# Performance work log

Measured on AMD Instinct MI355X. Metric: run time of the kernel, lower is better.

The kernel has to match this reference:

```python
import jax, jax.numpy as jnp
import numpy as np

BN_EPS = 1e-5


def setup_inputs() -> dict:
    key = jax.random.key(0)
    ks = jax.random.split(key, 9)
    C = 256
    x = jax.random.normal(ks[0], (4, C, 56, 56), jnp.float32)
    Wq = jax.random.normal(ks[1], (C // 4, C), jnp.float32) * 0.05
    Wk = jax.random.normal(ks[2], (C // 4, C), jnp.float32) * 0.05
    Wv = jax.random.normal(ks[3], (C, 2 * C), jnp.float32) * 0.05
    bv = jax.random.normal(ks[4], (C,), jnp.float32) * 0.05
    gamma = jnp.ones((C,), jnp.float32)
    beta = jnp.zeros((C,), jnp.float32)
    rmean = jax.random.normal(ks[5], (C,), jnp.float32) * 0.05
    rvar = jax.random.uniform(ks[6], (C,), jnp.float32) + 0.5
    return {"x": x, "Wq": Wq, "Wk": Wk, "Wv": Wv, "bv": bv,
            "gamma": gamma, "beta": beta, "rmean": rmean, "rvar": rvar, "k": 7}


def _patches(t, k):
    # t: [b, c, h, w] -> [b, c, k*k, h, w], zero-padded neighborhoods (matches F.unfold row-major order)
    b, c, h, w = t.shape
    p = (k - 1) // 2
    tp = jnp.pad(t, ((0, 0), (0, 0), (p, p), (p, p)))
    return jnp.stack([tp[:, :, i:i + h, j:j + w] for i in range(k) for j in range(k)], axis=2)


def _align(ta, tb, k, Wq, Wk):
    b, c, h, w = ta.shape
    hw = h * w
    # query token per pixel: [b, hw, 1, c]
    spta = ta.reshape(b, c, hw).transpose(0, 2, 1)[:, :, None, :]
    # unfolded k^2 neighborhood of tb: [b, hw, k2, c]
    pt = _patches(tb, k).reshape(b, c, k * k, hw).transpose(0, 3, 2, 1)
    keys = jnp.concatenate([spta, pt], axis=2)          # [b, hw, 1+k2, c]
    q = jnp.einsum('bnqc,dc->bnqd', spta, Wq)           # [b, hw, 1, c/4]
    kk = jnp.einsum('bnkc,dc->bnkd', keys, Wk)          # [b, hw, 1+k2, c/4]
    attn = jax.nn.softmax(jnp.einsum('bnqd,bnkd->bnqk', q, kk), axis=-1)
    out = jnp.einsum('bnqk,bnkc->bnqc', attn[..., 1:], pt)  # drop self-key column
    return out[:, :, 0, :].transpose(0, 2, 1).reshape(b, c, h, w)


def reference(x, Wq, Wk, Wv, bv, gamma, beta, rmean, rvar, k):
    xt1, xt2 = jnp.split(x, 2, axis=0)
    xt1 = _align(xt2, xt1, k, Wq, Wk)   # note: second call uses the freshly aligned xt1 (as in source)
    xt2 = _align(xt1, xt2, k, Wq, Wk)
    xt = jnp.concatenate([xt1, xt2], axis=0)
    cat = jnp.concatenate([x, xt], axis=1)              # [2B, 2C, H, W]
    y = jnp.einsum('bchw,oc->bohw', cat, Wv) + bv[None, :, None, None]
    scale = (gamma / jnp.sqrt(rvar + BN_EPS))[None, :, None, None]
    y = (y - rmean[None, :, None, None]) * scale + beta[None, :, None, None]
    return jax.nn.relu(y)
```

## Files before the change

### kernel.cpp

```cpp
#include <hip/hip_runtime.h>
#include <hip/hip_bf16.h>

#define HW 3136
#define W56 56

typedef __attribute__((ext_vector_type(8))) short short8;
typedef __attribute__((ext_vector_type(4))) float f32x4;

static __device__ __forceinline__ f32x4 mfma16(short8 a, short8 b, f32x4 c) {
    return __builtin_amdgcn_mfma_f32_16x16x32_bf16(a, b, c, 0, 0, 0);
}
static __device__ __forceinline__ float b2f(unsigned short u) {
    unsigned int x = ((unsigned int)u) << 16;
    return __builtin_bit_cast(float, x);
}
static __device__ __forceinline__ unsigned short f2b(float f) {
    __hip_bfloat16 h = __float2bfloat16(f);
    return *(unsigned short*)&h;
}

__global__ __launch_bounds__(256) void prep(const float* __restrict__ x,
                                            const float* __restrict__ Wq, const float* __restrict__ Wk,
                                            const float* __restrict__ Wv,
                                            unsigned short* __restrict__ catb,
                                            unsigned short* __restrict__ xlo,
                                            unsigned short* __restrict__ Wqk_hi,
                                            unsigned short* __restrict__ Wqk_lo,
                                            unsigned short* __restrict__ Wvb) {
    __shared__ float tile[32][33];
    int bx = blockIdx.x, tid = threadIdx.x;
    if (bx < 3136) {
        int b = bx / 784, rem = bx % 784;
        int p0 = (rem >> 3) * 32, c0 = (rem & 7) * 32;
        int tx = tid & 31, ty = tid >> 5;
#pragma unroll
        for (int i = ty; i < 32; i += 8)
            tile[i][tx] = x[((size_t)b * 256 + c0 + i) * HW + p0 + tx];
        __syncthreads();
#pragma unroll
        for (int i = ty; i < 32; i += 8) {
            float v = tile[tx][i];
            unsigned short hi = f2b(v);
            unsigned short lo = f2b(v - b2f(hi));
            size_t row = (size_t)b * HW + p0 + i;
            catb[row * 512 + c0 + tx] = hi;
            xlo[row * 256 + c0 + tx] = lo;
        }
    } else {
        int i = (bx - 3136) * 256 + tid;
        if (i < 32768) {
            float w = (i < 16384) ? Wq[i] : Wk[i - 16384];
            unsigned short hi = f2b(w);
            Wqk_hi[i] = hi;
            Wqk_lo[i] = f2b(w - b2f(hi));
        }
        if (i < 131072) Wvb[i] = f2b(Wv[i]);
    }
}

__global__ __launch_bounds__(256) void projqk(const unsigned short* __restrict__ Whi,
                                              const unsigned short* __restrict__ Wlo,
                                              const unsigned short* __restrict__ Bhi_g, int bstr,
                                              const unsigned short* __restrict__ Blo_g,
                                              float* __restrict__ Qout, float* __restrict__ Kout) {
    __shared__ short Ahi[64][72], Alo[64][72];
    __shared__ short Bhi[32][72], Blo[32][72];
    int tid = threadIdx.x, lane = tid & 63, wv = tid >> 6;
    int l15 = lane & 15, lk = (lane >> 4) * 8;
    int pxb = blockIdx.x * 32;
    int y64 = blockIdx.y * 64;
    f32x4 acc[2];
    acc[0] = (f32x4){0.f, 0.f, 0.f, 0.f};
    acc[1] = (f32x4){0.f, 0.f, 0.f, 0.f};

    for (int kt = 0; kt < 256; kt += 64) {
#pragma unroll
        for (int s = 0; s < 2; ++s) {
            int q = tid + 256 * s;
            int r = q >> 3, c = (q & 7) * 8;
            *(short8*)&Ahi[r][c] = *(const short8*)(Whi + (size_t)(y64 + r) * 256 + kt + c);
            *(short8*)&Alo[r][c] = *(const short8*)(Wlo + (size_t)(y64 + r) * 256 + kt + c);
        }
        {
            int r = tid >> 3, c = (tid & 7) * 8;
            *(short8*)&Bhi[r][c] = *(const short8*)(Bhi_g + (size_t)(pxb + r) * bstr + kt + c);
            *(short8*)&Blo[r][c] = *(const short8*)(Blo_g + (size_t)(pxb + r) * 256 + kt + c);
        }
        __syncthreads();
#pragma unroll
        for (int ks = 0; ks < 2; ++ks) {
            short8 ah = *(const short8*)&Ahi[wv * 16 + l15][ks * 32 + lk];
            short8 al = *(const short8*)&Alo[wv * 16 + l15][ks * 32 + lk];
            short8 bh[2], bl[2];
#pragma unroll
            for (int j = 0; j < 2; ++j) {
                bh[j] = *(const short8*)&Bhi[j * 16 + l15][ks * 32 + lk];
                bl[j] = *(const short8*)&Blo[j * 16 + l15][ks * 32 + lk];
            }
#pragma unroll
            for (int j = 0; j < 2; ++j) {
                acc[j] = mfma16(ah, bh[j], acc[j]);
                acc[j] = mfma16(ah, bl[j], acc[j]);
                acc[j] = mfma16(al, bh[j], acc[j]);
            }
        }
        __syncthreads();
    }
    int d0 = wv * 16 + (lane >> 4) * 4;
    float* base = blockIdx.y ? Kout : Qout;
#pragma unroll
    for (int j = 0; j < 2; ++j) {
        int px = pxb + j * 16 + l15;
        *(f32x4*)(base + (size_t)px * 64 + d0) = acc[j];
    }
}

__global__ __launch_bounds__(256) void attn_kernel(const float* __restrict__ Q,
                                                   const float* __restrict__ Kbase,
                                                   int selfOff, int kbOff,
                                                   const unsigned short* __restrict__ V,
                                                   unsigned short* __restrict__ outb,
                                                   unsigned short* __restrict__ outlo) {
    __shared__ float qs[4][64];
    __shared__ float wsh[4][64];
    __shared__ float ls[4][52];
    __shared__ int njsh[4][64];
    int tid = threadIdx.x, lane = tid & 63, wv = tid >> 6;
    int nbc = gridDim.x >> 3;
    int lb = (blockIdx.x & 7) * nbc + (blockIdx.x >> 3);
    int gw = lb * 4 + wv;
    int b = gw / HW, pix = gw % HW;
    int py = pix / W56, px = pix % W56;
    qs[wv][lane] = Q[(size_t)gw * 64 + lane];

    int valid = 0, nj = 0;
    if (lane == 0) {
        valid = 1;
    } else if (lane < 50) {
        int d = lane - 1, dy = d / 7 - 3, dx = d % 7 - 3;
        int ny = py + dy, nx = px + dx;
        if (ny >= 0 && ny < W56 && nx >= 0 && nx < W56) { valid = 1; nj = ny * W56 + nx; }
    }
    njsh[wv][lane] = nj;
    unsigned long long vmask = __ballot(lane < 50 && valid);
    __syncthreads();

    int rg = lane >> 4, c = lane & 15;
    f32x4 qf = *(const f32x4*)&qs[wv][c * 4];
    float4 kvv[13];
#pragma unroll
    for (int i = 0; i < 13; ++i) {
        int r = i * 4 + rg;
        int row = (i == 0 && rg == 0) ? (selfOff + gw) : (kbOff + b * HW + njsh[wv][r]);
        kvv[i] = *(const float4*)(Kbase + (size_t)row * 64 + c * 4);
    }
    float pl[13];
#pragma unroll
    for (int i = 0; i < 13; ++i)
        pl[i] = kvv[i].x * qf[0] + kvv[i].y * qf[1] + kvv[i].z * qf[2] + kvv[i].w * qf[3];
#pragma unroll
    for (int off = 1; off < 16; off <<= 1)
#pragma unroll
        for (int i = 0; i < 13; ++i) pl[i] += __shfl_xor(pl[i], off);
    float myl = 0.f;
#pragma unroll
    for (int i = 0; i < 13; ++i) myl = (c == i) ? pl[i] : myl;
    if (c < 13) ls[wv][c * 4 + rg] = myl;

    bool ok = (lane == 0) || (lane < 50 && ((vmask >> lane) & 1ull));
    float logit = (lane < 50 && ok) ? ls[wv][lane] : 0.f;
    float m = (lane < 50) ? logit : -1e30f;
#pragma unroll
    for (int off = 32; off; off >>= 1) m = fmaxf(m, __shfl_xor(m, off));
    float e = (lane < 50) ? __expf(logit - m) : 0.f;
    float s = e;
#pragma unroll
    for (int off = 32; off; off >>= 1) s += __shfl_xor(s, off);
    float w = (lane >= 1 && lane < 50 && valid) ? e / s : 0.f;
    wsh[wv][lane] = w;
    __syncthreads();

    int h = lane >> 5, l32 = lane & 31;
    int jb = h * 25;
    float av[8];
#pragma unroll
    for (int cc = 0; cc < 8; ++cc) av[cc] = 0.f;
    const unsigned short* vb = V + (size_t)b * HW * 512 + l32 * 8;
#pragma unroll
    for (int g = 0; g < 2; ++g) {
        float wj[12];
        short8 vj[12];
#pragma unroll
        for (int u = 0; u < 12; ++u) {
            int j = jb + g * 12 + u;
            wj[u] = wsh[wv][j];
            vj[u] = *(const short8*)(vb + (size_t)njsh[wv][j] * 512);
        }
#pragma unroll
        for (int u = 0; u < 12; ++u)
#pragma unroll
            for (int cc = 0; cc < 8; ++cc)
                av[cc] += wj[u] * b2f((unsigned short)vj[u][cc]);
    }
    {
        int j = jb + 24;
        float wt = wsh[wv][j];
        short8 vt = *(const short8*)(vb + (size_t)njsh[wv][j] * 512);
#pragma unroll
        for (int cc = 0; cc < 8; ++cc) av[cc] += wt * b2f((unsigned short)vt[cc]);
    }
#pragma unroll
    for (int cc = 0; cc < 8; ++cc) av[cc] += __shfl_xor(av[cc], 32);

    if (h == 0) {
        short8 pk, lo8;
#pragma unroll
        for (int cc = 0; cc < 8; ++cc) {
            unsigned short hi = f2b(av[cc]);
            pk[cc] = (short)hi;
            lo8[cc] = (short)f2b(av[cc] - b2f(hi));
        }
        *(short8*)(outb + (size_t)gw * 512 + l32 * 8) = pk;
        if (outlo) *(short8*)(outlo + (size_t)gw * 256 + l32 * 8) = lo8;
    }
}

__global__ __launch_bounds__(256) void conv_mfma(const unsigned short* __restrict__ catb,
                                                 const unsigned short* __restrict__ Wvb,
                                                 const float* __restrict__ bv, const float* __restrict__ gamma,
                                                 const float* __restrict__ beta, const float* __restrict__ rmean,
                                                 const float* __restrict__ rvar, float* __restrict__ out) {
    __shared__ short Ald[64][72];
    __shared__ short Bld[64][72];
    int tid = threadIdx.x, lane = tid & 63, wv = tid >> 6;
    int wm = wv >> 1, wn = wv & 1;
    int l15 = lane & 15, lk = (lane >> 4) * 8;
    int n0g = blockIdx.x * 64;
    int m0g = blockIdx.y * 64;
    f32x4 acc[2][2];
#pragma unroll
    for (int i = 0; i < 2; ++i)
#pragma unroll
        for (int j = 0; j < 2; ++j) acc[i][j] = (f32x4){0.f, 0.f, 0.f, 0.f};

    float sc_[2][4], sh_[2][4];
#pragma unroll
    for (int i = 0; i < 2; ++i) {
        int ob = m0g + wm * 32 + i * 16 + (lane >> 4) * 4;
#pragma unroll
        for (int r = 0; r < 4; ++r) {
            int o = ob + r;
            float s = gamma[o] * rsqrtf(rvar[o] + 1e-5f);
            sc_[i][r] = s;
            sh_[i][r] = (bv[o] - rmean[o]) * s + beta[o];
        }
    }

    for (int kt = 0; kt < 512; kt += 64) {
#pragma unroll
        for (int s = 0; s < 2; ++s) {
            int q = tid + 256 * s;
            int r = q >> 3, c = (q & 7) * 8;
            *(short8*)&Ald[r][c] = *(const short8*)(Wvb + (size_t)(m0g + r) * 512 + kt + c);
            *(short8*)&Bld[r][c] = *(const short8*)(catb + (size_t)(n0g + r) * 512 + kt + c);
        }
        __syncthreads();
#pragma unroll
        for (int ks = 0; ks < 2; ++ks) {
            short8 a[2], b[2];
#pragma unroll
            for (int i = 0; i < 2; ++i) a[i] = *(const short8*)&Ald[wm * 32 + i * 16 + l15][ks * 32 + lk];
#pragma unroll
            for (int j = 0; j < 2; ++j) b[j] = *(const short8*)&Bld[wn * 32 + j * 16 + l15][ks * 32 + lk];
#pragma unroll
            for (int i = 0; i < 2; ++i)
#pragma unroll
                for (int j = 0; j < 2; ++j) acc[i][j] = mfma16(a[i], b[j], acc[i][j]);
        }
        __syncthreads();
    }
#pragma unroll
    for (int i = 0; i < 2; ++i) {
        int ob = m0g + wm * 32 + i * 16 + (lane >> 4) * 4;
#pragma unroll
        for (int j = 0; j < 2; ++j) {
            int px = n0g + wn * 32 + j * 16 + l15;
            int b = px / HW, p = px - b * HW;
            f32x4 v = acc[i][j];
#pragma unroll
            for (int r = 0; r < 4; ++r) {
                out[((size_t)(b * 256 + ob + r)) * HW + p] = fmaxf(v[r] * sc_[i][r] + sh_[i][r], 0.f);
            }
        }
    }
}

extern "C" void kernel_launch(void* const* d_in, const int* in_sizes, int n_in,
                              void* d_out, int out_size, void* d_ws, size_t ws_size,
                              hipStream_t stream) {
    const float* x     = (const float*)d_in[0];
    const float* Wq    = (const float*)d_in[1];
    const float* Wk    = (const float*)d_in[2];
    const float* Wv    = (const float*)d_in[3];
    const float* bv    = (const float*)d_in[4];
    const float* gamma = (const float*)d_in[5];
    const float* beta  = (const float*)d_in[6];
    const float* rmean = (const float*)d_in[7];
    const float* rvar  = (const float*)d_in[8];
    float* out = (float*)d_out;

    float* Qall = (float*)d_ws;
    float* Kall = Qall + (size_t)4 * HW * 64;
    float* Qn   = Kall + (size_t)4 * HW * 64;
    float* Kn   = Qn + (size_t)2 * HW * 64;
    unsigned short* catb   = (unsigned short*)(Kn + (size_t)2 * HW * 64);
    unsigned short* xlo    = catb + (size_t)4 * HW * 512;
    unsigned short* xt1lo  = xlo + (size_t)4 * HW * 256;
    unsigned short* Wqk_hi = xt1lo + (size_t)2 * HW * 256;
    unsigned short* Wqk_lo = Wqk_hi + 128 * 256;
    unsigned short* Wvb    = Wqk_lo + 128 * 256;

    prep<<<3648, 256, 0, stream>>>(x, Wq, Wk, Wv, catb, xlo, Wqk_hi, Wqk_lo, Wvb);

    projqk<<<dim3(392, 2), 256, 0, stream>>>(Wqk_hi, Wqk_lo, catb, 512, xlo, Qall, Kall);

    attn_kernel<<<1568, 256, 0, stream>>>(Qall + (size_t)2 * HW * 64, Kall,
                                          2 * HW, 0,
                                          catb, catb + 256, xt1lo);

    projqk<<<dim3(196, 2), 256, 0, stream>>>(Wqk_hi, Wqk_lo, catb + 256, 512, xt1lo, Qn, Kn);

    attn_kernel<<<1568, 256, 0, stream>>>(Qn, Kall,
                                          6 * HW, 2 * HW,
                                          catb + (size_t)2 * HW * 512,
                                          catb + (size_t)2 * HW * 512 + 256, nullptr);

    conv_mfma<<<dim3(196, 4), 256, 0, stream>>>(catb, Wvb, bv, gamma, beta, rmean, rvar, out);
}
```

Measured before the change: 65.40 us.

## Stage shared V neighborhood tile in LDS for four adjacent pixels per block

Each block's four pixels are adjacent in a row, so their 7x7 neighborhoods are loaded once as a 7x10 tile of V rows into shared memory. The per-wave gathers then read from LDS instead of global memory. The Q staging in LDS and the first barrier are dropped, and the V loads are issued before the softmax to overlap latency. This costs about 35 KB of LDS per block, which may reduce occupancy.

```diff
diff --git a/kernel.cpp b/kernel.cpp
--- a/kernel.cpp
+++ b/kernel.cpp
@@ -121,32 +121,37 @@
                                                    const unsigned short* __restrict__ V,
                                                    unsigned short* __restrict__ outb,
                                                    unsigned short* __restrict__ outlo) {
-    __shared__ float qs[4][64];
+    __shared__ unsigned short Vs[70 * 256];
     __shared__ float wsh[4][64];
     __shared__ float ls[4][52];
     __shared__ int njsh[4][64];
+    __shared__ int slotsh[4][64];
     int tid = threadIdx.x, lane = tid & 63, wv = tid >> 6;
     int nbc = gridDim.x >> 3;
     int lb = (blockIdx.x & 7) * nbc + (blockIdx.x >> 3);
-    int gw = lb * 4 + wv;
-    int b = gw / HW, pix = gw % HW;
-    int py = pix / W56, px = pix % W56;
-    qs[wv][lane] = Q[(size_t)gw * 64 + lane];
-
-    int valid = 0, nj = 0;
+    int pixg = lb * 4;
+    int b = pixg / HW, pix0 = pixg % HW;
+    int row0 = pix0 / W56, px0 = pix0 % W56;
+    int gw = pixg + wv;
+    int py = row0, px = px0 + wv;
+
+    int valid = 0, nj = 0, slot = 0;
     if (lane == 0) {
         valid = 1;
     } else if (lane < 50) {
         int d = lane - 1, dy = d / 7 - 3, dx = d % 7 - 3;
         int ny = py + dy, nx = px + dx;
-        if (ny >= 0 && ny < W56 && nx >= 0 && nx < W56) { valid = 1; nj = ny * W56 + nx; }
+        if (ny >= 0 && ny < W56 && nx >= 0 && nx < W56) {
+            valid = 1;
+            nj = ny * W56 + nx;
+            slot = (dy + 3) * 10 + (wv + dx + 3);
+        }
     }
     njsh[wv][lane] = nj;
-    unsigned long long vmask = __ballot(lane < 50 && valid);
-    __syncthreads();
+    slotsh[wv][lane] = slot;
 
     int rg = lane >> 4, c = lane & 15;
-    f32x4 qf = *(const f32x4*)&qs[wv][c * 4];
+    f32x4 qf = *(const f32x4*)(Q + (size_t)gw * 64 + c * 4);
     float4 kvv[13];
 #pragma unroll
     for (int i = 0; i < 13; ++i) {
@@ -154,6 +159,21 @@
         int row = (i == 0 && rg == 0) ? (selfOff + gw) : (kbOff + b * HW + njsh[wv][r]);
         kvv[i] = *(const float4*)(Kbase + (size_t)row * 64 + c * 4);
     }
+
+    const unsigned short* Vb = V + (size_t)b * HW * 512;
+    short8 svj[9];
+#pragma unroll
+    for (int it = 0; it < 9; ++it) {
+        int item = it * 256 + tid;
+        if (item < 2240) {
+            int urow = item >> 5, sl = item & 31;
+            int r = urow / 10, cc = urow % 10;
+            int ny = row0 - 3 + r, nx = px0 - 3 + cc;
+            int unj = (ny >= 0 && ny < W56 && nx >= 0 && nx < W56) ? (ny * W56 + nx) : 0;
+            svj[it] = *(const short8*)(Vb + (size_t)unj * 512 + sl * 8);
+        }
+    }
+
     float pl[13];
 #pragma unroll
     for (int i = 0; i < 13; ++i)
@@ -167,8 +187,7 @@
     for (int i = 0; i < 13; ++i) myl = (c == i) ? pl[i] : myl;
     if (c < 13) ls[wv][c * 4 + rg] = myl;
 
-    bool ok = (lane == 0) || (lane < 50 && ((vmask >> lane) & 1ull));
-    float logit = (lane < 50 && ok) ? ls[wv][lane] : 0.f;
+    float logit = (lane < 50 && valid) ? ls[wv][lane] : 0.f;
     float m = (lane < 50) ? logit : -1e30f;
 #pragma unroll
     for (int off = 32; off; off >>= 1) m = fmaxf(m, __shfl_xor(m, off));
@@ -178,6 +197,15 @@
     for (int off = 32; off; off >>= 1) s += __shfl_xor(s, off);
     float w = (lane >= 1 && lane < 50 && valid) ? e / s : 0.f;
     wsh[wv][lane] = w;
+
+#pragma unroll
+    for (int it = 0; it < 9; ++it) {
+        int item = it * 256 + tid;
+        if (item < 2240) {
+            int urow = item >> 5, sl = item & 31;
+            *(short8*)&Vs[urow * 256 + sl * 8] = svj[it];
+        }
+    }
     __syncthreads();
 
     int h = lane >> 5, l32 = lane & 31;
@@ -185,7 +213,6 @@
     float av[8];
 #pragma unroll
     for (int cc = 0; cc < 8; ++cc) av[cc] = 0.f;
-    const unsigned short* vb = V + (size_t)b * HW * 512 + l32 * 8;
 #pragma unroll
     for (int g = 0; g < 2; ++g) {
         float wj[12];
@@ -194,7 +221,7 @@
         for (int u = 0; u < 12; ++u) {
             int j = jb + g * 12 + u;
             wj[u] = wsh[wv][j];
-            vj[u] = *(const short8*)(vb + (size_t)njsh[wv][j] * 512);
+            vj[u] = *(const short8*)&Vs[slotsh[wv][j] * 256 + l32 * 8];
         }
 #pragma unroll
         for (int u = 0; u < 12; ++u)
@@ -205,7 +232,7 @@
     {
         int j = jb + 24;
         float wt = wsh[wv][j];
-        short8 vt = *(const short8*)(vb + (size_t)njsh[wv][j] * 512);
+        short8 vt = *(const short8*)&Vs[slotsh[wv][j] * 256 + l32 * 8];
 #pragma unroll
         for (int cc = 0; cc < 8; ++cc) av[cc] += wt * b2f((unsigned short)vt[cc]);
     }
```

Result: slower. 68.34 us (+4.5%).

## Store K projections as bf16, prefetch projqk tiles, drop attn block barriers

Applied to the files above, without the earlier changes.

The K projection output is now written as bf16 instead of fp32, and the attention kernel gathers these half-size rows for the 49-neighbour dot products. This halves the bytes moved by the main gather. projqk now prefetches the next K-tile into registers while the MFMAs run on the current shared-memory tile. The attention kernel reads Q straight from global memory and drops its two __syncthreads, relying on each wave touching only its own shared rows. Rounding K to bf16 reduces logit precision, which may slightly change the softmax weights.

```diff
diff --git a/kernel.cpp b/kernel.cpp
--- a/kernel.cpp
+++ b/kernel.cpp
@@ -62,31 +62,42 @@
                                               const unsigned short* __restrict__ Wlo,
                                               const unsigned short* __restrict__ Bhi_g, int bstr,
                                               const unsigned short* __restrict__ Blo_g,
-                                              float* __restrict__ Qout, float* __restrict__ Kout) {
+                                              float* __restrict__ Qout,
+                                              unsigned short* __restrict__ Kout) {
     __shared__ short Ahi[64][72], Alo[64][72];
     __shared__ short Bhi[32][72], Blo[32][72];
     int tid = threadIdx.x, lane = tid & 63, wv = tid >> 6;
     int l15 = lane & 15, lk = (lane >> 4) * 8;
     int pxb = blockIdx.x * 32;
     int y64 = blockIdx.y * 64;
+    int ar0 = tid >> 3, ac = (tid & 7) * 8;
+    int br = tid >> 3, bc = (tid & 7) * 8;
     f32x4 acc[2];
     acc[0] = (f32x4){0.f, 0.f, 0.f, 0.f};
     acc[1] = (f32x4){0.f, 0.f, 0.f, 0.f};
 
-    for (int kt = 0; kt < 256; kt += 64) {
-#pragma unroll
-        for (int s = 0; s < 2; ++s) {
-            int q = tid + 256 * s;
-            int r = q >> 3, c = (q & 7) * 8;
-            *(short8*)&Ahi[r][c] = *(const short8*)(Whi + (size_t)(y64 + r) * 256 + kt + c);
-            *(short8*)&Alo[r][c] = *(const short8*)(Wlo + (size_t)(y64 + r) * 256 + kt + c);
-        }
-        {
-            int r = tid >> 3, c = (tid & 7) * 8;
-            *(short8*)&Bhi[r][c] = *(const short8*)(Bhi_g + (size_t)(pxb + r) * bstr + kt + c);
-            *(short8*)&Blo[r][c] = *(const short8*)(Blo_g + (size_t)(pxb + r) * 256 + kt + c);
-        }
-        __syncthreads();
+    short8 rAh0 = *(const short8*)(Whi + (size_t)(y64 + ar0) * 256 + ac);
+    short8 rAl0 = *(const short8*)(Wlo + (size_t)(y64 + ar0) * 256 + ac);
+    short8 rAh1 = *(const short8*)(Whi + (size_t)(y64 + ar0 + 32) * 256 + ac);
+    short8 rAl1 = *(const short8*)(Wlo + (size_t)(y64 + ar0 + 32) * 256 + ac);
+    short8 rBh  = *(const short8*)(Bhi_g + (size_t)(pxb + br) * bstr + bc);
+    short8 rBl  = *(const short8*)(Blo_g + (size_t)(pxb + br) * 256 + bc);
+
+#pragma unroll
+    for (int t = 0; t < 4; ++t) {
+        *(short8*)&Ahi[ar0][ac] = rAh0;      *(short8*)&Alo[ar0][ac] = rAl0;
+        *(short8*)&Ahi[ar0 + 32][ac] = rAh1; *(short8*)&Alo[ar0 + 32][ac] = rAl1;
+        *(short8*)&Bhi[br][bc] = rBh;        *(short8*)&Blo[br][bc] = rBl;
+        __syncthreads();
+        if (t < 3) {
+            int kn = t * 64 + 64;
+            rAh0 = *(const short8*)(Whi + (size_t)(y64 + ar0) * 256 + kn + ac);
+            rAl0 = *(const short8*)(Wlo + (size_t)(y64 + ar0) * 256 + kn + ac);
+            rAh1 = *(const short8*)(Whi + (size_t)(y64 + ar0 + 32) * 256 + kn + ac);
+            rAl1 = *(const short8*)(Wlo + (size_t)(y64 + ar0 + 32) * 256 + kn + ac);
+            rBh  = *(const short8*)(Bhi_g + (size_t)(pxb + br) * bstr + kn + bc);
+            rBl  = *(const short8*)(Blo_g + (size_t)(pxb + br) * 256 + kn + bc);
+        }
 #pragma unroll
         for (int ks = 0; ks < 2; ++ks) {
             short8 ah = *(const short8*)&Ahi[wv * 16 + l15][ks * 32 + lk];
@@ -107,21 +118,30 @@
         __syncthreads();
     }
     int d0 = wv * 16 + (lane >> 4) * 4;
-    float* base = blockIdx.y ? Kout : Qout;
-#pragma unroll
-    for (int j = 0; j < 2; ++j) {
-        int px = pxb + j * 16 + l15;
-        *(f32x4*)(base + (size_t)px * 64 + d0) = acc[j];
+    if (blockIdx.y == 0) {
+#pragma unroll
+        for (int j = 0; j < 2; ++j) {
+            int px = pxb + j * 16 + l15;
+            *(f32x4*)(Qout + (size_t)px * 64 + d0) = acc[j];
+        }
+    } else {
+#pragma unroll
+        for (int j = 0; j < 2; ++j) {
+            int px = pxb + j * 16 + l15;
+            ushort4 kb;
+            kb.x = f2b(acc[j][0]); kb.y = f2b(acc[j][1]);
+            kb.z = f2b(acc[j][2]); kb.w = f2b(acc[j][3]);
+            *(ushort4*)(Kout + (size_t)px * 64 + d0) = kb;
+        }
     }
 }
 
 __global__ __launch_bounds__(256) void attn_kernel(const float* __restrict__ Q,
-                                                   const float* __restrict__ Kbase,
+                                                   const unsigned short* __restrict__ Kb,
                                                    int selfOff, int kbOff,
                                                    const unsigned short* __restrict__ V,
                                                    unsigned short* __restrict__ outb,
                                                    unsigned short* __restrict__ outlo) {
-    __shared__ float qs[4][64];
     __shared__ float wsh[4][64];
     __shared__ float ls[4][52];
     __shared__ int njsh[4][64];
@@ -131,7 +151,6 @@
     int gw = lb * 4 + wv;
     int b = gw / HW, pix = gw % HW;
     int py = pix / W56, px = pix % W56;
-    qs[wv][lane] = Q[(size_t)gw * 64 + lane];
 
     int valid = 0, nj = 0;
     if (lane == 0) {
@@ -142,22 +161,22 @@
         if (ny >= 0 && ny < W56 && nx >= 0 && nx < W56) { valid = 1; nj = ny * W56 + nx; }
     }
     njsh[wv][lane] = nj;
-    unsigned long long vmask = __ballot(lane < 50 && valid);
-    __syncthreads();
 
     int rg = lane >> 4, c = lane & 15;
-    f32x4 qf = *(const f32x4*)&qs[wv][c * 4];
-    float4 kvv[13];
+    f32x4 qf = *(const f32x4*)(Q + (size_t)gw * 64 + c * 4);
+    ushort4 kvv[13];
 #pragma unroll
     for (int i = 0; i < 13; ++i) {
         int r = i * 4 + rg;
         int row = (i == 0 && rg == 0) ? (selfOff + gw) : (kbOff + b * HW + njsh[wv][r]);
-        kvv[i] = *(const float4*)(Kbase + (size_t)row * 64 + c * 4);
-    }
+        kvv[i] = *(const ushort4*)(Kb + (size_t)row * 64 + c * 4);
+    }
+
     float pl[13];
 #pragma unroll
     for (int i = 0; i < 13; ++i)
-        pl[i] = kvv[i].x * qf[0] + kvv[i].y * qf[1] + kvv[i].z * qf[2] + kvv[i].w * qf[3];
+        pl[i] = b2f(kvv[i].x) * qf[0] + b2f(kvv[i].y) * qf[1] +
+                b2f(kvv[i].z) * qf[2] + b2f(kvv[i].w) * qf[3];
 #pragma unroll
     for (int off = 1; off < 16; off <<= 1)
 #pragma unroll
@@ -167,8 +186,7 @@
     for (int i = 0; i < 13; ++i) myl = (c == i) ? pl[i] : myl;
     if (c < 13) ls[wv][c * 4 + rg] = myl;
 
-    bool ok = (lane == 0) || (lane < 50 && ((vmask >> lane) & 1ull));
-    float logit = (lane < 50 && ok) ? ls[wv][lane] : 0.f;
+    float logit = (lane < 50 && valid) ? ls[wv][lane] : 0.f;
     float m = (lane < 50) ? logit : -1e30f;
 #pragma unroll
     for (int off = 32; off; off >>= 1) m = fmaxf(m, __shfl_xor(m, off));
@@ -178,7 +196,6 @@
     for (int off = 32; off; off >>= 1) s += __shfl_xor(s, off);
     float w = (lane >= 1 && lane < 50 && valid) ? e / s : 0.f;
     wsh[wv][lane] = w;
-    __syncthreads();
 
     int h = lane >> 5, l32 = lane & 31;
     int jb = h * 25;
@@ -310,10 +327,9 @@
     float* out = (float*)d_out;
 
     float* Qall = (float*)d_ws;
-    float* Kall = Qall + (size_t)4 * HW * 64;
-    float* Qn   = Kall + (size_t)4 * HW * 64;
-    float* Kn   = Qn + (size_t)2 * HW * 64;
-    unsigned short* catb   = (unsigned short*)(Kn + (size_t)2 * HW * 64);
+    float* Qn   = Qall + (size_t)4 * HW * 64;
+    unsigned short* Kb = (unsigned short*)(Qn + (size_t)2 * HW * 64);
+    unsigned short* catb   = Kb + (size_t)6 * HW * 64;
     unsigned short* xlo    = catb + (size_t)4 * HW * 512;
     unsigned short* xt1lo  = xlo + (size_t)4 * HW * 256;
     unsigned short* Wqk_hi = xt1lo + (size_t)2 * HW * 256;
@@ -322,16 +338,17 @@
 
     prep<<<3648, 256, 0, stream>>>(x, Wq, Wk, Wv, catb, xlo, Wqk_hi, Wqk_lo, Wvb);
 
-    projqk<<<dim3(392, 2), 256, 0, stream>>>(Wqk_hi, Wqk_lo, catb, 512, xlo, Qall, Kall);
-
-    attn_kernel<<<1568, 256, 0, stream>>>(Qall + (size_t)2 * HW * 64, Kall,
+    projqk<<<dim3(392, 2), 256, 0, stream>>>(Wqk_hi, Wqk_lo, catb, 512, xlo, Qall, Kb);
+
+    attn_kernel<<<1568, 256, 0, stream>>>(Qall + (size_t)2 * HW * 64, Kb,
                                           2 * HW, 0,
                                           catb, catb + 256, xt1lo);
 
-    projqk<<<dim3(196, 2), 256, 0, stream>>>(Wqk_hi, Wqk_lo, catb + 256, 512, xt1lo, Qn, Kn);
-
-    attn_kernel<<<1568, 256, 0, stream>>>(Qn, Kall,
-                                          6 * HW, 2 * HW,
+    projqk<<<dim3(196, 2), 256, 0, stream>>>(Wqk_hi, Wqk_lo, catb + 256, 512, xt1lo,
+                                             Qn, Kb + (size_t)4 * HW * 64);
+
+    attn_kernel<<<1568, 256, 0, stream>>>(Qn, Kb,
+                                          4 * HW, 2 * HW,
                                           catb + (size_t)2 * HW * 512,
                                           catb + (size_t)2 * HW * 512 + 256, nullptr);
 
```

New measurement: 62.90 us. 1.04x faster.
